# Performance work log

Hardware: AMD Instinct MI355X
Metric: run time of the kernel (lower is better)

The kernel has to match this reference:

```python
import jax, jax.numpy as jnp
import numpy as np

HEADS = 16
NU = 1
EPS = 1e-6


def dpfp(k):
    """Deterministic Parameter-Free Projection, normalized. k: [..., d_k] -> [..., 2*d_k*NU]."""
    x = jax.nn.relu(jnp.concatenate([k, -k], axis=-1))  # [..., 2*d_k]
    x_rolled = jnp.concatenate([jnp.roll(x, i, axis=-1) for i in range(1, NU + 1)], axis=-1)
    x_repeat = jnp.concatenate([x] * NU, axis=-1)
    phi = x_repeat * x_rolled
    return phi / (jnp.sum(phi, axis=-1, keepdims=True) + EPS)


def setup_inputs() -> dict:
    key = jax.random.key(0)
    ks = jax.random.split(key, 7)
    S, B, D, H = 4096, 4, 1024, HEADS
    scale = 0.02
    return {
        "x": jax.random.normal(ks[0], (S, B, D), dtype=jnp.float32),
        "Wq": jax.random.normal(ks[1], (D, D), dtype=jnp.float32) * scale,
        "Wk": jax.random.normal(ks[2], (D, D), dtype=jnp.float32) * scale,
        "Wv": jax.random.normal(ks[3], (D, D), dtype=jnp.float32) * scale,
        "Wb": jax.random.normal(ks[4], (D, H), dtype=jnp.float32) * scale,
        "Wo": jax.random.normal(ks[5], (D, D), dtype=jnp.float32) * scale,
        "bo": jnp.zeros((D,), dtype=jnp.float32),
    }


def reference(x, Wq, Wk, Wv, Wb, Wo, bo):
    S, B, D = x.shape
    H = HEADS
    dk = D // H
    d_dot = 2 * dk * NU

    # Projections: [S, B, H, d_k] (bias-free linears + head split)
    q = dpfp((x @ Wq).reshape(S, B, H, dk))   # [S, B, H, d_dot]
    k = dpfp((x @ Wk).reshape(S, B, H, dk))   # [S, B, H, d_dot]
    v = (x @ Wv).reshape(S, B, H, dk)          # [S, B, H, d_k]
    beta = jax.nn.sigmoid(x @ Wb).reshape(S, B, H, 1)  # [S, B, H, 1]

    W0 = jnp.zeros((B, H, dk, d_dot), dtype=x.dtype)  # fast-weight state

    def step(W, inputs):
        k_i, v_i, q_i, b_i = inputs  # [B,H,d_dot], [B,H,dk], [B,H,d_dot], [B,H,1]
        v_bar = jnp.einsum('bhvk,bhk->bhv', W, k_i)
        W = W + jnp.einsum('bhv,bhk->bhvk', b_i * (v_i - v_bar), k_i)
        y = jnp.einsum('bhvk,bhk->bhv', W, q_i)  # [B, H, dk]
        return W, y.reshape(B, H * dk)

    _, outputs = jax.lax.scan(step, W0, (k, v, q, beta))  # [S, B, D]
    return outputs @ Wo + bo
```

## Files before the change

kernel.cpp:

```cpp
#include <hip/hip_runtime.h>

#define S_LEN 4096
#define BATCH 4
#define NROWS 16384
#define DIM   1024
#define CHUNK 32
#define NCHUNK (S_LEN / CHUNK)

typedef __attribute__((ext_vector_type(8))) short short8;
typedef __attribute__((ext_vector_type(4))) float floatx4;
typedef _Float16 half_t;
typedef __attribute__((ext_vector_type(8))) _Float16 half8;

__device__ __forceinline__ float bf2f(short s) {
    union { unsigned int u; float f; } c;
    c.u = ((unsigned int)(unsigned short)s) << 16;
    return c.f;
}
__device__ __forceinline__ short f2bf(float f) {
    union { float f; unsigned int u; } c; c.f = f;
    unsigned int r = c.u + 0x7fffu + ((c.u >> 16) & 1u);
    return (short)(r >> 16);
}
__device__ __forceinline__ void split_bf16(float x, short& hi, short& lo) {
    short h = f2bf(x);
    hi = h;
    lo = f2bf(x - bf2f(h));
}

__device__ __forceinline__ float row16_allreduce(float x) {
    union fi { float f; int i; };
    fi a, b;
    a.f = x;
    b.i = __builtin_amdgcn_update_dpp(0, a.i, 0xB1,  0xF, 0xF, true); a.f += b.f;
    b.i = __builtin_amdgcn_update_dpp(0, a.i, 0x4E,  0xF, 0xF, true); a.f += b.f;
    b.i = __builtin_amdgcn_update_dpp(0, a.i, 0x124, 0xF, 0xF, true); a.f += b.f;
    b.i = __builtin_amdgcn_update_dpp(0, a.i, 0x128, 0xF, 0xF, true); a.f += b.f;
    return a.f;
}

__global__ __launch_bounds__(256) void transpose_k(const float* __restrict__ W,
                                                   float* __restrict__ Wt,
                                                   int K, int N) {
    int idx = blockIdx.x * 256 + threadIdx.x;
    if (idx >= N * K) return;
    int n = idx / K;
    int k = idx - n * K;
    Wt[idx] = W[k * N + n];
}

template <typename AT, int MODE>
__global__ __launch_bounds__(256) void gemm_bt(const AT* __restrict__ A,
                                               const float* __restrict__ Bt,
                                               void* __restrict__ Cout,
                                               const float* __restrict__ bias,
                                               int N, int K) {
    __shared__ __align__(16) short As_h[128][40], As_l[128][40];
    __shared__ __align__(16) short Bs_h[128][40], Bs_l[128][40];
    const int tid  = threadIdx.x;
    const int wave = tid >> 6, lane = tid & 63;
    const int wr = wave >> 1, wc = wave & 1;
    const int row0 = blockIdx.x * 128, col0 = blockIdx.y * 128;
    const int lr = tid >> 1, lc = (tid & 1) * 16;
    const AT*    Ap = A  + (size_t)(row0 + lr) * K + lc;
    const float* Bp = Bt + (size_t)(col0 + lr) * K + lc;
    const int fr = lane & 15;
    const int ak = (lane >> 4) * 8;
    floatx4 acc[4][4];
    #pragma unroll
    for (int m = 0; m < 4; ++m)
        #pragma unroll
        for (int n = 0; n < 4; ++n) acc[m][n] = (floatx4){0.f, 0.f, 0.f, 0.f};

    for (int k0 = 0; k0 < K; k0 += 32) {
        float av[16], bv[16];
        if constexpr (sizeof(AT) == 4) {
            #pragma unroll
            for (int g = 0; g < 4; ++g) {
                floatx4 a = *(const floatx4*)(Ap + k0 + g * 4);
                #pragma unroll
                for (int j = 0; j < 4; ++j) av[g * 4 + j] = a[j];
            }
        } else {
            #pragma unroll
            for (int g = 0; g < 2; ++g) {
                half8 a = *(const half8*)(Ap + k0 + g * 8);
                #pragma unroll
                for (int j = 0; j < 8; ++j) av[g * 8 + j] = (float)a[j];
            }
        }
        #pragma unroll
        for (int g = 0; g < 4; ++g) {
            floatx4 v = *(const floatx4*)(Bp + k0 + g * 4);
            #pragma unroll
            for (int j = 0; j < 4; ++j) bv[g * 4 + j] = v[j];
        }

        short8 ah[2], al[2], bh[2], bl[2];
        #pragma unroll
        for (int g = 0; g < 2; ++g)
            #pragma unroll
            for (int j = 0; j < 8; ++j) {
                short h, l;
                split_bf16(av[g * 8 + j], h, l); ah[g][j] = h; al[g][j] = l;
                split_bf16(bv[g * 8 + j], h, l); bh[g][j] = h; bl[g][j] = l;
            }
        #pragma unroll
        for (int g = 0; g < 2; ++g) {
            *(short8*)&As_h[lr][lc + g * 8] = ah[g];
            *(short8*)&As_l[lr][lc + g * 8] = al[g];
            *(short8*)&Bs_h[lr][lc + g * 8] = bh[g];
            *(short8*)&Bs_l[lr][lc + g * 8] = bl[g];
        }
        __syncthreads();

        short8 afh[4], afl[4], bfh[4], bfl[4];
        #pragma unroll
        for (int m = 0; m < 4; ++m) {
            afh[m] = *(const short8*)&As_h[wr * 64 + m * 16 + fr][ak];
            afl[m] = *(const short8*)&As_l[wr * 64 + m * 16 + fr][ak];
        }
        #pragma unroll
        for (int n = 0; n < 4; ++n) {
            bfh[n] = *(const short8*)&Bs_h[wc * 64 + n * 16 + fr][ak];
            bfl[n] = *(const short8*)&Bs_l[wc * 64 + n * 16 + fr][ak];
        }
        #pragma unroll
        for (int m = 0; m < 4; ++m)
            #pragma unroll
            for (int n = 0; n < 4; ++n) {
                acc[m][n] = __builtin_amdgcn_mfma_f32_16x16x32_bf16(afh[m], bfh[n], acc[m][n], 0, 0, 0);
                acc[m][n] = __builtin_amdgcn_mfma_f32_16x16x32_bf16(afh[m], bfl[n], acc[m][n], 0, 0, 0);
                acc[m][n] = __builtin_amdgcn_mfma_f32_16x16x32_bf16(afl[m], bfh[n], acc[m][n], 0, 0, 0);
            }
        __syncthreads();
    }
    #pragma unroll
    for (int m = 0; m < 4; ++m) {
        const int crow = row0 + wr * 64 + m * 16 + (lane >> 4) * 4;
        #pragma unroll
        for (int n = 0; n < 4; ++n) {
            const int col = col0 + wc * 64 + n * 16 + (lane & 15);
            #pragma unroll
            for (int r = 0; r < 4; ++r) {
                int row = crow + r;
                float v = acc[m][n][r];
                if (MODE == 0) {
                    float bb = bias ? bias[col] : 0.f;
                    ((float*)Cout)[(size_t)row * N + col] = v + bb;
                } else {
                    ((half_t*)Cout)[(size_t)row * 2048 + (col >> 6) * 128 + (col & 63)] = (half_t)v;
                }
            }
        }
    }
}

__global__ __launch_bounds__(256) void beta_kernel(const float* __restrict__ X,
                                                   const float* __restrict__ Wbt,
                                                   float* __restrict__ Beta) {
    int wid  = (blockIdx.x * 256 + threadIdx.x) >> 6;
    int lane = threadIdx.x & 63;
    if (wid >= NROWS) return;
    const float* xr = X + (size_t)wid * DIM + lane * 16;
    float xv[16];
    #pragma unroll
    for (int j = 0; j < 4; ++j) {
        floatx4 v = *(const floatx4*)(xr + j * 4);
        #pragma unroll
        for (int e = 0; e < 4; ++e) xv[j * 4 + e] = v[e];
    }
    #pragma unroll 1
    for (int h = 0; h < 16; ++h) {
        const float* wr = Wbt + h * DIM + lane * 16;
        float s = 0.f;
        #pragma unroll
        for (int j = 0; j < 4; ++j) {
            floatx4 v = *(const floatx4*)(wr + j * 4);
            #pragma unroll
            for (int e = 0; e < 4; ++e) s = fmaf(xv[j * 4 + e], v[e], s);
        }
        #pragma unroll
        for (int off = 32; off; off >>= 1) s += __shfl_xor(s, off);
        if (lane == 0) Beta[wid * 16 + h] = 1.f / (1.f + __expf(-s));
    }
}

__global__ __launch_bounds__(256) void dpfp_h(half_t* __restrict__ P) {
    int gw   = (blockIdx.x * 256 + threadIdx.x) >> 6;
    int lane = threadIdx.x & 63;
    half_t* base = P + (size_t)gw * 128;
    float p  = (float)base[lane];
    float pm = __shfl(p, (lane + 63) & 63);
    float rp  = fmaxf(p, 0.f),  rn  = fmaxf(-p, 0.f);
    float rpm = fmaxf(pm, 0.f), rnm = fmaxf(-pm, 0.f);
    float aprev = (lane == 0) ? rnm : rpm;
    float bprev = (lane == 0) ? rpm : rnm;
    float phi_a = rp * aprev;
    float phi_b = rn * bprev;
    float s = phi_a + phi_b;
    #pragma unroll
    for (int off = 32; off; off >>= 1) s += __shfl_xor(s, off);
    float inv = 1.f / (s + 1e-6f);
    base[lane]      = (half_t)(phi_a * inv);
    base[64 + lane] = (half_t)(phi_b * inv);
}


#define LOADSTEP(DK, DQ, STEP)                                              \
    {                                                                       \
        floatx4 _ka = *(const floatx4*)&Ks[bufi][STEP][tc * 8];             \
        floatx4 _kb = *(const floatx4*)&Ks[bufi][STEP][tc * 8 + 4];         \
        floatx4 _qa = *(const floatx4*)&Qs[bufi][STEP][tc * 8];             \
        floatx4 _qb = *(const floatx4*)&Qs[bufi][STEP][tc * 8 + 4];         \
        for (int _i = 0; _i < 4; ++_i) {                                    \
            DK[_i] = _ka[_i]; DK[4 + _i] = _kb[_i];                         \
            DQ[_i] = _qa[_i]; DQ[4 + _i] = _qb[_i];                         \
        }                                                                   \
    }

#define DOT8(RES, X, Y)                                                     \
    {                                                                       \
        float _s0 = X[0] * Y[0], _s1 = X[1] * Y[1];                         \
        _s0 = fmaf(X[2], Y[2], _s0); _s1 = fmaf(X[3], Y[3], _s1);           \
        _s0 = fmaf(X[4], Y[4], _s0); _s1 = fmaf(X[5], Y[5], _s1);           \
        _s0 = fmaf(X[6], Y[6], _s0); _s1 = fmaf(X[7], Y[7], _s1);           \
        RES = _s0 + _s1;                                                    \
    }

#define PAIR(CEK, CEQ, COK, COQ, CEV, CEB, COV, COB, CG,                    \
             NEK, NEQ, NOK, NOQ, NEV, NEB, NOV, NOB, NG, P)                 \
    {                                                                       \
        if ((P) + 1 < 16) {                                                 \
            LOADSTEP(NEK, NEQ, 2 * (P) + 2);                                \
            LOADSTEP(NOK, NOQ, 2 * (P) + 3);                                \
            NEV = Vs[bufi][2 * (P) + 2][row_l];                             \
            NEB = Bs[bufi][2 * (P) + 2];                                    \
            NOV = Vs[bufi][2 * (P) + 3][row_l];                             \
            NOB = Bs[bufi][2 * (P) + 3];                                    \
            NG  = *(const floatx4*)&GramLDS[(P) + 1][0];                    \
        }                                                                   \
        float _e0, _e1, _f0, _f1;                                           \
        DOT8(_e0, w, CEK); DOT8(_e1, w, COK);                               \
        DOT8(_f0, w, CEQ); DOT8(_f1, w, COQ);                               \
        _e0 = row16_allreduce(_e0); _e1 = row16_allreduce(_e1);             \
        _f0 = row16_allreduce(_f0); _f1 = row16_allreduce(_f1);             \
        float _c0 = CEB * (CEV - _e0);                                      \
        float _d1 = fmaf(_c0, CG[0], _e1);                                  \
        float _c1 = COB * (COV - _d1);                                      \
        float _y0 = fmaf(_c0, CG[1], _f0);                                  \
        float _y1 = fmaf(_c1, CG[3], fmaf(_c0, CG[2], _f1));                \
        for (int _j = 0; _j < 8; ++_j)                                      \
            w[_j] = fmaf(_c1, COK[_j], fmaf(_c0, CEK[_j], w[_j]));          \
        if (tc == 0) {                                                      \
            ybase[(size_t)((cc * CHUNK + 2 * (P))     * BATCH + b) * 1024] = (half_t)_y0; \
            ybase[(size_t)((cc * CHUNK + 2 * (P) + 1) * BATCH + b) * 1024] = (half_t)_y1; \
        }                                                                   \
    }

__global__ __launch_bounds__(256, 1) void scan_kernel(const half_t* __restrict__ PhiK,
                                                      const half_t* __restrict__ PhiQ,
                                                      const float* __restrict__ V,
                                                      const float* __restrict__ Beta,
                                                      half_t* __restrict__ Y) {
    __shared__ float Ks[2][CHUNK][128];
    __shared__ float Qs[2][CHUNK][128];
    __shared__ float Vs[2][CHUNK][16];
    __shared__ float Bs[2][CHUNK];
    __shared__ float GramLDS[16][4];

    const int bh = blockIdx.x >> 2;
    const int rc = blockIdx.x & 3;
    const int b = bh >> 4, h = bh & 15;
    const int tid = threadIdx.x;
    const int row_l = tid >> 4;
    const int tc = tid & 15;
    const int vrow = rc * 16 + row_l;

    const half_t* kg = PhiK + h * 128;
    const half_t* qg = PhiQ + h * 128;
    const float*  vg = V + h * 64 + rc * 16;
    const float*  bg = Beta + h;
    half_t* ybase = Y + h * 64 + vrow;

    {
        #pragma unroll
        for (int rpt = 0; rpt < 2; ++rpt) {
            int i = rpt * 256 + tid;
            int st = i >> 4, seg = i & 15, row = i & 15;
            size_t r = (size_t)(st * BATCH + b);
            half8 kv = *(const half8*)(kg + r * 2048 + seg * 8);
            half8 qv = *(const half8*)(qg + r * 2048 + seg * 8);
            floatx4 klo, khi, qlo, qhi;
            #pragma unroll
            for (int j = 0; j < 4; ++j) {
                klo[j] = (float)kv[j]; khi[j] = (float)kv[4 + j];
                qlo[j] = (float)qv[j]; qhi[j] = (float)qv[4 + j];
            }
            *(floatx4*)&Ks[0][st][seg * 8]     = klo;
            *(floatx4*)&Ks[0][st][seg * 8 + 4] = khi;
            *(floatx4*)&Qs[0][st][seg * 8]     = qlo;
            *(floatx4*)&Qs[0][st][seg * 8 + 4] = qhi;
            Vs[0][st][row] = vg[r * 1024 + row];
        }
        if (tid < CHUNK) {
            size_t r = (size_t)(tid * BATCH + b);
            Bs[0][tid] = bg[r * 16];
        }
    }
    __syncthreads();

    float w[8];
    #pragma unroll
    for (int j = 0; j < 8; ++j) w[j] = 0.f;

    for (int cc = 0; cc < NCHUNK; ++cc) {
        const int bufi = cc & 1;
        const bool more = (cc + 1 < NCHUNK);

        {
            float ka[8], kb[8], qa[8], qb[8];
            LOADSTEP(ka, qa, 2 * row_l);
            LOADSTEP(kb, qb, 2 * row_l + 1);
            float skk, s00, s01, s11;
            DOT8(skk, ka, kb);
            DOT8(s00, ka, qa);
            DOT8(s01, ka, qb);
            DOT8(s11, kb, qb);
            skk = row16_allreduce(skk);
            s00 = row16_allreduce(s00);
            s01 = row16_allreduce(s01);
            s11 = row16_allreduce(s11);
            if (tc == 0) {
                GramLDS[row_l][0] = skk;
                GramLDS[row_l][1] = s00;
                GramLDS[row_l][2] = s01;
                GramLDS[row_l][3] = s11;
            }
        }
        __syncthreads();

        half8 pk[2], pq[2];
        float pv[2], pb = 0.f;
        if (more) {
            #pragma unroll
            for (int rpt = 0; rpt < 2; ++rpt) {
                int i = rpt * 256 + tid;
                int st = i >> 4, seg = i & 15, row = i & 15;
                size_t r = (size_t)(((cc + 1) * CHUNK + st) * BATCH + b);
                pk[rpt] = *(const half8*)(kg + r * 2048 + seg * 8);
                pq[rpt] = *(const half8*)(qg + r * 2048 + seg * 8);
                pv[rpt] = vg[r * 1024 + row];
            }
            if (tid < CHUNK) {
                size_t r = (size_t)(((cc + 1) * CHUNK + tid) * BATCH + b);
                pb = bg[r * 16];
            }
        }

        float EK0[8], EQ0[8], OK0[8], OQ0[8];
        float EK1[8], EQ1[8], OK1[8], OQ1[8];
        float Ev0, Eb0, Ov0, Ob0, Ev1, Eb1, Ov1, Ob1;
        floatx4 G0, G1;
        LOADSTEP(EK0, EQ0, 0);
        LOADSTEP(OK0, OQ0, 1);
        Ev0 = Vs[bufi][0][row_l]; Eb0 = Bs[bufi][0];
        Ov0 = Vs[bufi][1][row_l]; Ob0 = Bs[bufi][1];
        G0 = *(const floatx4*)&GramLDS[0][0];

        #pragma unroll 1
        for (int p2 = 0; p2 < 16; p2 += 2) {
            PAIR(EK0, EQ0, OK0, OQ0, Ev0, Eb0, Ov0, Ob0, G0,
                 EK1, EQ1, OK1, OQ1, Ev1, Eb1, Ov1, Ob1, G1, p2);
            PAIR(EK1, EQ1, OK1, OQ1, Ev1, Eb1, Ov1, Ob1, G1,
                 EK0, EQ0, OK0, OQ0, Ev0, Eb0, Ov0, Ob0, G0, p2 + 1);
        }

        if (more) {
            const int bufn = bufi ^ 1;
            #pragma unroll
            for (int rpt = 0; rpt < 2; ++rpt) {
                int i = rpt * 256 + tid;
                int st = i >> 4, seg = i & 15, row = i & 15;
                floatx4 klo, khi, qlo, qhi;
                #pragma unroll
                for (int j = 0; j < 4; ++j) {
                    klo[j] = (float)pk[rpt][j]; khi[j] = (float)pk[rpt][4 + j];
                    qlo[j] = (float)pq[rpt][j]; qhi[j] = (float)pq[rpt][4 + j];
                }
                *(floatx4*)&Ks[bufn][st][seg * 8]     = klo;
                *(floatx4*)&Ks[bufn][st][seg * 8 + 4] = khi;
                *(floatx4*)&Qs[bufn][st][seg * 8]     = qlo;
                *(floatx4*)&Qs[bufn][st][seg * 8 + 4] = qhi;
                Vs[bufn][st][row] = pv[rpt];
            }
            if (tid < CHUNK) Bs[bufn][tid] = pb;
        }
        __syncthreads();
    }
}

extern "C" void kernel_launch(void* const* d_in, const int* in_sizes, int n_in,
                              void* d_out, int out_size, void* d_ws, size_t ws_size,
                              hipStream_t stream) {
    const float* x  = (const float*)d_in[0];
    const float* Wq = (const float*)d_in[1];
    const float* Wk = (const float*)d_in[2];
    const float* Wv = (const float*)d_in[3];
    const float* Wb = (const float*)d_in[4];
    const float* Wo = (const float*)d_in[5];
    const float* bo = (const float*)d_in[6];

    char* ws = (char*)d_ws;
    size_t off = 0;
    auto alloc = [&](size_t bytes) -> void* {
        void* p = ws + off;
        off += (bytes + 255) & ~(size_t)255;
        return p;
    };
    half_t* PhiQ = (half_t*)alloc((size_t)NROWS * 2048 * 2);
    half_t* PhiK = (half_t*)alloc((size_t)NROWS * 2048 * 2);
    half_t* Yb   = (half_t*)alloc((size_t)NROWS * 1024 * 2);
    float*  Beta = (float*)alloc((size_t)NROWS * 16 * 4);
    float*  Wqt  = (float*)alloc((size_t)1024 * 1024 * 4);
    float*  Wkt  = (float*)alloc((size_t)1024 * 1024 * 4);
    float*  Wvt  = (float*)alloc((size_t)1024 * 1024 * 4);
    float*  Wot  = (float*)alloc((size_t)1024 * 1024 * 4);
    float*  Wbt  = (float*)alloc((size_t)16 * 1024 * 4);
    float*  Vb   = (float*)d_out;

    transpose_k<<<4096, 256, 0, stream>>>(Wq, Wqt, 1024, 1024);
    transpose_k<<<4096, 256, 0, stream>>>(Wk, Wkt, 1024, 1024);
    transpose_k<<<4096, 256, 0, stream>>>(Wv, Wvt, 1024, 1024);
    transpose_k<<<4096, 256, 0, stream>>>(Wo, Wot, 1024, 1024);
    transpose_k<<<64,   256, 0, stream>>>(Wb, Wbt, 1024, 16);

    dim3 ggrid(NROWS / 128, DIM / 128);
    const int dgrid = (NROWS * 16) / 4;
    gemm_bt<float, 1><<<ggrid, 256, 0, stream>>>(x, Wqt, PhiQ, nullptr, DIM, DIM);
    dpfp_h<<<dgrid, 256, 0, stream>>>(PhiQ);
    gemm_bt<float, 1><<<ggrid, 256, 0, stream>>>(x, Wkt, PhiK, nullptr, DIM, DIM);
    dpfp_h<<<dgrid, 256, 0, stream>>>(PhiK);
    gemm_bt<float, 0><<<ggrid, 256, 0, stream>>>(x, Wvt, Vb, nullptr, DIM, DIM);
    beta_kernel<<<NROWS / 4, 256, 0, stream>>>(x, Wbt, Beta);
    scan_kernel<<<256, 256, 0, stream>>>(PhiK, PhiQ, Vb, Beta, Yb);
    gemm_bt<half_t, 0><<<ggrid, 256, 0, stream>>>(Yb, Wot, d_out, bo, DIM, DIM);
}
```

Before: 1.454 ms.

## Pre-split fp32 operands into bf16 hi/lo buffers before GEMMs

```diff
diff --git a/kernel.cpp b/kernel.cpp
--- a/kernel.cpp
+++ b/kernel.cpp
@@ -49,9 +49,57 @@
     Wt[idx] = W[k * N + n];
 }
 
-template <typename AT, int MODE>
-__global__ __launch_bounds__(256) void gemm_bt(const AT* __restrict__ A,
-                                               const float* __restrict__ Bt,
+__global__ __launch_bounds__(256) void transpose_split(const float* __restrict__ W,
+                                                       short* __restrict__ Wth,
+                                                       short* __restrict__ Wtl,
+                                                       int K, int N) {
+    int idx = blockIdx.x * 256 + threadIdx.x;
+    if (idx >= N * K) return;
+    int n = idx / K;
+    int k = idx - n * K;
+    short h, l;
+    split_bf16(W[k * N + n], h, l);
+    Wth[idx] = h;
+    Wtl[idx] = l;
+}
+
+__global__ __launch_bounds__(256) void split_f32(const float* __restrict__ X,
+                                                 short* __restrict__ Xh,
+                                                 short* __restrict__ Xl) {
+    size_t idx = ((size_t)blockIdx.x * 256 + threadIdx.x) * 8;
+    floatx4 a = *(const floatx4*)(X + idx);
+    floatx4 b = *(const floatx4*)(X + idx + 4);
+    short8 h, l;
+    #pragma unroll
+    for (int j = 0; j < 4; ++j) {
+        short hh, ll;
+        split_bf16(a[j], hh, ll); h[j] = hh; l[j] = ll;
+        split_bf16(b[j], hh, ll); h[4 + j] = hh; l[4 + j] = ll;
+    }
+    *(short8*)(Xh + idx) = h;
+    *(short8*)(Xl + idx) = l;
+}
+
+__global__ __launch_bounds__(256) void split_f16(const half_t* __restrict__ X,
+                                                 short* __restrict__ Xh,
+                                                 short* __restrict__ Xl) {
+    size_t idx = ((size_t)blockIdx.x * 256 + threadIdx.x) * 8;
+    half8 a = *(const half8*)(X + idx);
+    short8 h, l;
+    #pragma unroll
+    for (int j = 0; j < 8; ++j) {
+        short hh, ll;
+        split_bf16((float)a[j], hh, ll); h[j] = hh; l[j] = ll;
+    }
+    *(short8*)(Xh + idx) = h;
+    *(short8*)(Xl + idx) = l;
+}
+
+template <int MODE>
+__global__ __launch_bounds__(256) void gemm_sb(const short* __restrict__ Ah,
+                                               const short* __restrict__ Al,
+                                               const short* __restrict__ Bh,
+                                               const short* __restrict__ Bl,
                                                void* __restrict__ Cout,
                                                const float* __restrict__ bias,
                                                int N, int K) {
@@ -62,8 +110,10 @@
     const int wr = wave >> 1, wc = wave & 1;
     const int row0 = blockIdx.x * 128, col0 = blockIdx.y * 128;
     const int lr = tid >> 1, lc = (tid & 1) * 16;
-    const AT*    Ap = A  + (size_t)(row0 + lr) * K + lc;
-    const float* Bp = Bt + (size_t)(col0 + lr) * K + lc;
+    const short* Aph = Ah + (size_t)(row0 + lr) * K + lc;
+    const short* Apl = Al + (size_t)(row0 + lr) * K + lc;
+    const short* Bph = Bh + (size_t)(col0 + lr) * K + lc;
+    const short* Bpl = Bl + (size_t)(col0 + lr) * K + lc;
     const int fr = lane & 15;
     const int ak = (lane >> 4) * 8;
     floatx4 acc[4][4];
@@ -73,45 +123,22 @@
         for (int n = 0; n < 4; ++n) acc[m][n] = (floatx4){0.f, 0.f, 0.f, 0.f};
 
     for (int k0 = 0; k0 < K; k0 += 32) {
-        float av[16], bv[16];
-        if constexpr (sizeof(AT) == 4) {
-            #pragma unroll
-            for (int g = 0; g < 4; ++g) {
-                floatx4 a = *(const floatx4*)(Ap + k0 + g * 4);
-                #pragma unroll
-                for (int j = 0; j < 4; ++j) av[g * 4 + j] = a[j];
-            }
-        } else {
-            #pragma unroll
-            for (int g = 0; g < 2; ++g) {
-                half8 a = *(const half8*)(Ap + k0 + g * 8);
-                #pragma unroll
-                for (int j = 0; j < 8; ++j) av[g * 8 + j] = (float)a[j];
-            }
-        }
-        #pragma unroll
-        for (int g = 0; g < 4; ++g) {
-            floatx4 v = *(const floatx4*)(Bp + k0 + g * 4);
-            #pragma unroll
-            for (int j = 0; j < 4; ++j) bv[g * 4 + j] = v[j];
-        }
-
-        short8 ah[2], al[2], bh[2], bl[2];
-        #pragma unroll
-        for (int g = 0; g < 2; ++g)
-            #pragma unroll
-            for (int j = 0; j < 8; ++j) {
-                short h, l;
-                split_bf16(av[g * 8 + j], h, l); ah[g][j] = h; al[g][j] = l;
-                split_bf16(bv[g * 8 + j], h, l); bh[g][j] = h; bl[g][j] = l;
-            }
-        #pragma unroll
-        for (int g = 0; g < 2; ++g) {
-            *(short8*)&As_h[lr][lc + g * 8] = ah[g];
-            *(short8*)&As_l[lr][lc + g * 8] = al[g];
-            *(short8*)&Bs_h[lr][lc + g * 8] = bh[g];
-            *(short8*)&Bs_l[lr][lc + g * 8] = bl[g];
-        }
+        short8 vah0 = *(const short8*)(Aph + k0);
+        short8 vah1 = *(const short8*)(Aph + k0 + 8);
+        short8 val0 = *(const short8*)(Apl + k0);
+        short8 val1 = *(const short8*)(Apl + k0 + 8);
+        short8 vbh0 = *(const short8*)(Bph + k0);
+        short8 vbh1 = *(const short8*)(Bph + k0 + 8);
+        short8 vbl0 = *(const short8*)(Bpl + k0);
+        short8 vbl1 = *(const short8*)(Bpl + k0 + 8);
+        *(short8*)&As_h[lr][lc]     = vah0;
+        *(short8*)&As_h[lr][lc + 8] = vah1;
+        *(short8*)&As_l[lr][lc]     = val0;
+        *(short8*)&As_l[lr][lc + 8] = val1;
+        *(short8*)&Bs_h[lr][lc]     = vbh0;
+        *(short8*)&Bs_h[lr][lc + 8] = vbh1;
+        *(short8*)&Bs_l[lr][lc]     = vbl0;
+        *(short8*)&Bs_l[lr][lc + 8] = vbl1;
         __syncthreads();
 
         short8 afh[4], afl[4], bfh[4], bfl[4];
@@ -422,27 +449,35 @@
     half_t* PhiK = (half_t*)alloc((size_t)NROWS * 2048 * 2);
     half_t* Yb   = (half_t*)alloc((size_t)NROWS * 1024 * 2);
     float*  Beta = (float*)alloc((size_t)NROWS * 16 * 4);
-    float*  Wqt  = (float*)alloc((size_t)1024 * 1024 * 4);
-    float*  Wkt  = (float*)alloc((size_t)1024 * 1024 * 4);
-    float*  Wvt  = (float*)alloc((size_t)1024 * 1024 * 4);
-    float*  Wot  = (float*)alloc((size_t)1024 * 1024 * 4);
+    short*  Xh   = (short*)alloc((size_t)NROWS * 1024 * 2);
+    short*  Xl   = (short*)alloc((size_t)NROWS * 1024 * 2);
+    short*  Wqh  = (short*)alloc((size_t)1024 * 1024 * 2);
+    short*  Wql  = (short*)alloc((size_t)1024 * 1024 * 2);
+    short*  Wkh  = (short*)alloc((size_t)1024 * 1024 * 2);
+    short*  Wkl  = (short*)alloc((size_t)1024 * 1024 * 2);
+    short*  Wvh  = (short*)alloc((size_t)1024 * 1024 * 2);
+    short*  Wvl  = (short*)alloc((size_t)1024 * 1024 * 2);
+    short*  Woh  = (short*)alloc((size_t)1024 * 1024 * 2);
+    short*  Wol  = (short*)alloc((size_t)1024 * 1024 * 2);
     float*  Wbt  = (float*)alloc((size_t)16 * 1024 * 4);
     float*  Vb   = (float*)d_out;
 
-    transpose_k<<<4096, 256, 0, stream>>>(Wq, Wqt, 1024, 1024);
-    transpose_k<<<4096, 256, 0, stream>>>(Wk, Wkt, 1024, 1024);
-    transpose_k<<<4096, 256, 0, stream>>>(Wv, Wvt, 1024, 1024);
-    transpose_k<<<4096, 256, 0, stream>>>(Wo, Wot, 1024, 1024);
-    transpose_k<<<64,   256, 0, stream>>>(Wb, Wbt, 1024, 16);
+    transpose_split<<<4096, 256, 0, stream>>>(Wq, Wqh, Wql, 1024, 1024);
+    transpose_split<<<4096, 256, 0, stream>>>(Wk, Wkh, Wkl, 1024, 1024);
+    transpose_split<<<4096, 256, 0, stream>>>(Wv, Wvh, Wvl, 1024, 1024);
+    transpose_split<<<4096, 256, 0, stream>>>(Wo, Woh, Wol, 1024, 1024);
+    transpose_k<<<64, 256, 0, stream>>>(Wb, Wbt, 1024, 16);
+    split_f32<<<8192, 256, 0, stream>>>(x, Xh, Xl);
 
     dim3 ggrid(NROWS / 128, DIM / 128);
     const int dgrid = (NROWS * 16) / 4;
-    gemm_bt<float, 1><<<ggrid, 256, 0, stream>>>(x, Wqt, PhiQ, nullptr, DIM, DIM);
+    gemm_sb<1><<<ggrid, 256, 0, stream>>>(Xh, Xl, Wqh, Wql, PhiQ, nullptr, DIM, DIM);
     dpfp_h<<<dgrid, 256, 0, stream>>>(PhiQ);
-    gemm_bt<float, 1><<<ggrid, 256, 0, stream>>>(x, Wkt, PhiK, nullptr, DIM, DIM);
+    gemm_sb<1><<<ggrid, 256, 0, stream>>>(Xh, Xl, Wkh, Wkl, PhiK, nullptr, DIM, DIM);
     dpfp_h<<<dgrid, 256, 0, stream>>>(PhiK);
-    gemm_bt<float, 0><<<ggrid, 256, 0, stream>>>(x, Wvt, Vb, nullptr, DIM, DIM);
+    gemm_sb<0><<<ggrid, 256, 0, stream>>>(Xh, Xl, Wvh, Wvl, Vb, nullptr, DIM, DIM);
     beta_kernel<<<NROWS / 4, 256, 0, stream>>>(x, Wbt, Beta);
     scan_kernel<<<256, 256, 0, stream>>>(PhiK, PhiQ, Vb, Beta, Yb);
-    gemm_bt<half_t, 0><<<ggrid, 256, 0, stream>>>(Yb, Wot, d_out, bo, DIM, DIM);
-}
+    split_f16<<<8192, 256, 0, stream>>>(Yb, Xh, Xl);
+    gemm_sb<0><<<ggrid, 256, 0, stream>>>(Xh, Xl, Woh, Wol, d_out, bo, DIM, DIM);
+}
```

Result: no change. 1.438 ms (-1.1%).
